# Kernel optimization log

Measured on AMD Instinct MI355X. Metric: run time of the kernel, lower is better.

Reference implementation:

```python
import jax, jax.numpy as jnp
import numpy as np
from jax import lax

B = 4096
SRC = 50   # source_seq_len (encoder runs SRC-1 steps)
TGT = 25   # target_seq_len
R = 1024   # rnn_size
H = 67     # HUMAN_SIZE
I = 82     # input_size = 67 + 15 one-hot actions


def gru_cell(x, h, Wi, Wh, bi, bh):
    # torch.nn.GRUCell semantics; gate order (r, z, n); Wi:[3R,in], Wh:[3R,R]
    gi = x @ Wi.T + bi
    gh = h @ Wh.T + bh
    ir, iz, inn = jnp.split(gi, 3, axis=1)
    hr, hz, hn = jnp.split(gh, 3, axis=1)
    r = jax.nn.sigmoid(ir + hr)
    z = jax.nn.sigmoid(iz + hz)
    n = jnp.tanh(inn + r * hn)
    return (1.0 - z) * n + z * h


def setup_inputs() -> dict:
    key = jax.random.key(0)
    ks = jax.random.split(key, 12)
    s = 0.05
    return {
        "encoder_inputs": jax.random.normal(ks[0], (B, SRC - 1, I), jnp.float32),
        "decoder_inputs": jax.random.normal(ks[1], (B, TGT, I), jnp.float32),
        "Wi1": jax.random.normal(ks[2], (3 * R, I), jnp.float32) * s,
        "Wh1": jax.random.normal(ks[3], (3 * R, R), jnp.float32) * s,
        "bi1": jax.random.normal(ks[4], (3 * R,), jnp.float32) * s,
        "bh1": jax.random.normal(ks[5], (3 * R,), jnp.float32) * s,
        "Wi2": jax.random.normal(ks[6], (3 * R, R), jnp.float32) * s,
        "Wh2": jax.random.normal(ks[7], (3 * R, R), jnp.float32) * s,
        "bi2": jax.random.normal(ks[8], (3 * R,), jnp.float32) * s,
        "bh2": jax.random.normal(ks[9], (3 * R,), jnp.float32) * s,
        "Wfc": jax.random.normal(ks[10], (H, 2 * R), jnp.float32) * s,
        "bfc": jax.random.normal(ks[11], (H,), jnp.float32) * s,
        "use_cuda": 0,
    }


def reference(encoder_inputs, decoder_inputs, Wi1, Wh1, bi1, bh1,
              Wi2, Wh2, bi2, bh2, Wfc, bfc, use_cuda):
    # dropout=0.0 / eval mode -> dropout is identity (faithful to module defaults)
    bsz = encoder_inputs.shape[0]
    enc = jnp.transpose(encoder_inputs, (1, 0, 2))  # [SRC-1, B, I]
    dec = jnp.transpose(decoder_inputs, (1, 0, 2))  # [TGT,   B, I]

    s1 = jnp.zeros((bsz, R), encoder_inputs.dtype)
    s2 = jnp.zeros((bsz, R), encoder_inputs.dtype)

    def enc_step(carry, x):
        s1, s2 = carry
        s1 = gru_cell(x, s1, Wi1, Wh1, bi1, bh1)
        s2 = gru_cell(s1, s2, Wi2, Wh2, bi2, bh2)
        return (s1, s2), None

    (s1, s2), _ = lax.scan(enc_step, (s1, s2), enc)

    # decoder feeds back previous output (loop_function = identity on prev)
    prev0 = dec[0][:, :H]

    def dec_step(carry, dec_t):
        s1, s2, prev = carry
        inp = lax.stop_gradient(jnp.concatenate([prev, dec_t[:, H:]], axis=1))  # .detach()
        s1 = gru_cell(inp, s1, Wi1, Wh1, bi1, bh1)
        s2 = gru_cell(s1, s2, Wi2, Wh2, bi2, bh2)
        state_out = jnp.concatenate([s1, s2], axis=1)          # [B, 2R]
        out = inp[:, :H] + state_out @ Wfc.T + bfc             # residual velocities
        return (s1, s2, out), out

    _, outputs = lax.scan(dec_step, (s1, s2, prev0), dec)      # [TGT, B, H]
    return jnp.transpose(outputs, (1, 0, 2))                   # [B, TGT, H]
```

## Files before the change

### kernel.cpp

```cpp
#include <hip/hip_runtime.h>
#include <hip/hip_bf16.h>
#include <math.h>

#define B_        4096
#define ENC_STEPS 49
#define TGT_      25
#define R_        1024
#define H_        67
#define I_        82
#define IP_       96
#define IP2_      192
#define NG_       3072
#define FCN_      128
#define K2_       2048

typedef unsigned short u16;
typedef __attribute__((ext_vector_type(8))) short bf16x8_t;
typedef __attribute__((ext_vector_type(4))) float f32x4_t;

__device__ __forceinline__ float bf2f(u16 h) {
    union { unsigned int u; float f; } v; v.u = ((unsigned int)h) << 16; return v.f;
}
__device__ __forceinline__ u16 f2bf(float f) {
    union { unsigned int u; float f; } v; v.f = f;
    unsigned int u = v.u;
    u += 0x7fffu + ((u >> 16) & 1u);
    return (u16)(u >> 16);
}
__device__ __forceinline__ float sigmf(float x) { return 1.f / (1.f + __expf(-x)); }
__device__ __forceinline__ float tanhfast(float x) { return 1.f - 2.f / (__expf(2.f * x) + 1.f); }

__device__ __forceinline__ void g2l16(const u16* g, u16* l) {
    __builtin_amdgcn_global_load_lds(
        (const __attribute__((address_space(1))) unsigned int*)(const void*)g,
        (__attribute__((address_space(3))) unsigned int*)(void*)l,
        16, 0, 0);
}

__global__ void cast_bf16_kernel(const float* __restrict__ s, u16* __restrict__ d, int n) {
    int i = blockIdx.x * 256 + threadIdx.x;
    if (i < n) d[i] = f2bf(s[i]);
}
__global__ void pad_wi1_dup_kernel(const float* __restrict__ s, u16* __restrict__ d) {
    int i = blockIdx.x * 256 + threadIdx.x;
    if (i >= NG_ * IP2_) return;
    int r = i / IP2_, c = i % IP2_;
    int cc = (c < IP_) ? c : c - IP_;
    d[i] = (cc < I_) ? f2bf(s[r * I_ + cc]) : (u16)0;
}
__global__ void pad_wfc_kernel(const float* __restrict__ s, u16* __restrict__ d) {
    int i = blockIdx.x * 256 + threadIdx.x;
    if (i >= FCN_ * K2_) return;
    int r = i / K2_, c = i % K2_;
    d[i] = (r < H_) ? f2bf(s[r * K2_ + c]) : (u16)0;
}

__global__ void pad_all_x_kernel(const float* __restrict__ enc, u16* __restrict__ xall) {
    int i = blockIdx.x * 256 + threadIdx.x;
    if (i >= B_ * ENC_STEPS * IP_) return;
    int c = i % IP_;
    int t = (i / IP_) % ENC_STEPS;
    int b = i / (IP_ * ENC_STEPS);
    float v = (c < I_) ? enc[((size_t)b * ENC_STEPS + t) * I_ + c] : 0.f;
    u16 hi = f2bf(v);
    u16 lo = f2bf(v - bf2f(hi));
    size_t base = ((size_t)t * B_ + b) * IP2_;
    xall[base + c]       = hi;
    xall[base + IP_ + c] = lo;
}

__global__ void build_inp_kernel(const float* __restrict__ prev, int pstride,
                                 const float* __restrict__ dec, int t,
                                 u16* __restrict__ xpad) {
    int i = blockIdx.x * 256 + threadIdx.x;
    if (i >= B_ * IP_) return;
    int b = i / IP_, c = i % IP_;
    float v = 0.f;
    if (c < H_)      v = prev[(size_t)b * pstride + c];
    else if (c < I_) v = dec[((size_t)b * TGT_ + t) * I_ + c];
    u16 hi = f2bf(v);
    u16 lo = f2bf(v - bf2f(hi));
    xpad[(size_t)b * IP2_ + c]       = hi;
    xpad[(size_t)b * IP2_ + IP_ + c] = lo;
}

template<int KX>
__global__ __launch_bounds__(256, 2) void gru_step_kernel(
    const u16* __restrict__ Ax, int ldax,
    const u16* __restrict__ Wx,
    const u16* __restrict__ Ah, int ldah,
    const u16* __restrict__ Wh,
    const float* __restrict__ bi, const float* __restrict__ bh,
    float* __restrict__ hf,
    u16* __restrict__ hout)
{
    __shared__ __align__(16) u16 As[128 * 32];
    __shared__ __align__(16) u16 Ws[3 * 64 * 32];

    const int tid  = threadIdx.x;
    const int lane = tid & 63, wave = tid >> 6;
    const int wm = wave >> 1, wn = wave & 1;
    const int mbase = blockIdx.y * 128;
    const int nbase = blockIdx.x * 64;
    const int lr = lane & 15;
    const int sw = (((lane >> 4) ^ (lr & 3)) * 8);

    f32x4_t acc_r[4][2], acc_z[4][2], acc_xn[4][2], acc_hn[4][2];
#pragma unroll
    for (int i = 0; i < 4; i++)
#pragma unroll
        for (int j = 0; j < 2; j++) {
            acc_r[i][j]  = (f32x4_t){0,0,0,0};
            acc_z[i][j]  = (f32x4_t){0,0,0,0};
            acc_xn[i][j] = (f32x4_t){0,0,0,0};
            acc_hn[i][j] = (f32x4_t){0,0,0,0};
        }

    for (int k0 = 0; k0 < KX; k0 += 32) {
        __syncthreads();
#pragma unroll
        for (int p = 0; p < 2; p++) {
            int g = tid + p * 256;
            int row = g >> 2;
            int ch  = (g & 3) ^ (row & 3);
            g2l16(Ax + (size_t)(mbase + row) * ldax + k0 + ch * 8, As + g * 8);
        }
#pragma unroll
        for (int p = 0; p < 3; p++) {
            int q = tid + p * 256;
            int gate = q >> 8, rg = (q >> 2) & 63, cw = (q & 3) ^ (rg & 3);
            g2l16(Wx + ((size_t)gate * R_ + nbase + rg) * KX + k0 + cw * 8, Ws + q * 8);
        }
        __syncthreads();
        bf16x8_t a_f[4], w_r[2], w_z[2], w_n[2];
#pragma unroll
        for (int i = 0; i < 4; i++)
            a_f[i] = *(const bf16x8_t*)(As + (wm * 64 + i * 16 + lr) * 32 + sw);
#pragma unroll
        for (int j = 0; j < 2; j++) {
            int c = wn * 32 + j * 16 + lr;
            w_r[j] = *(const bf16x8_t*)(Ws + c * 32 + sw);
            w_z[j] = *(const bf16x8_t*)(Ws + (64 + c) * 32 + sw);
            w_n[j] = *(const bf16x8_t*)(Ws + (128 + c) * 32 + sw);
        }
#pragma unroll
        for (int i = 0; i < 4; i++)
#pragma unroll
            for (int j = 0; j < 2; j++) {
                acc_r[i][j]  = __builtin_amdgcn_mfma_f32_16x16x32_bf16(a_f[i], w_r[j], acc_r[i][j], 0, 0, 0);
                acc_z[i][j]  = __builtin_amdgcn_mfma_f32_16x16x32_bf16(a_f[i], w_z[j], acc_z[i][j], 0, 0, 0);
                acc_xn[i][j] = __builtin_amdgcn_mfma_f32_16x16x32_bf16(a_f[i], w_n[j], acc_xn[i][j], 0, 0, 0);
            }
    }

    for (int k0 = 0; k0 < R_; k0 += 32) {
        __syncthreads();
#pragma unroll
        for (int p = 0; p < 2; p++) {
            int g = tid + p * 256;
            int row = g >> 2;
            int ch  = (g & 3) ^ (row & 3);
            g2l16(Ah + (size_t)(mbase + row) * ldah + k0 + ch * 8, As + g * 8);
        }
#pragma unroll
        for (int p = 0; p < 3; p++) {
            int q = tid + p * 256;
            int gate = q >> 8, rg = (q >> 2) & 63, cw = (q & 3) ^ (rg & 3);
            g2l16(Wh + ((size_t)gate * R_ + nbase + rg) * R_ + k0 + cw * 8, Ws + q * 8);
        }
        __syncthreads();
        bf16x8_t a_f[4], w_r[2], w_z[2], w_n[2];
#pragma unroll
        for (int i = 0; i < 4; i++)
            a_f[i] = *(const bf16x8_t*)(As + (wm * 64 + i * 16 + lr) * 32 + sw);
#pragma unroll
        for (int j = 0; j < 2; j++) {
            int c = wn * 32 + j * 16 + lr;
            w_r[j] = *(const bf16x8_t*)(Ws + c * 32 + sw);
            w_z[j] = *(const bf16x8_t*)(Ws + (64 + c) * 32 + sw);
            w_n[j] = *(const bf16x8_t*)(Ws + (128 + c) * 32 + sw);
        }
#pragma unroll
        for (int i = 0; i < 4; i++)
#pragma unroll
            for (int j = 0; j < 2; j++) {
                acc_r[i][j]  = __builtin_amdgcn_mfma_f32_16x16x32_bf16(a_f[i], w_r[j], acc_r[i][j], 0, 0, 0);
                acc_z[i][j]  = __builtin_amdgcn_mfma_f32_16x16x32_bf16(a_f[i], w_z[j], acc_z[i][j], 0, 0, 0);
                acc_hn[i][j] = __builtin_amdgcn_mfma_f32_16x16x32_bf16(a_f[i], w_n[j], acc_hn[i][j], 0, 0, 0);
            }
    }

    const int rr2 = (lane >> 4) * 4;
#pragma unroll
    for (int j = 0; j < 2; j++) {
        const int col = nbase + wn * 32 + j * 16 + lr;
        const float b_ir = bi[col],          b_hr = bh[col];
        const float b_iz = bi[R_ + col],     b_hz = bh[R_ + col];
        const float b_in = bi[2 * R_ + col], b_hn = bh[2 * R_ + col];
#pragma unroll
        for (int i = 0; i < 4; i++) {
#pragma unroll
            for (int r = 0; r < 4; r++) {
                const int row = mbase + wm * 64 + i * 16 + rr2 + r;
                const float hold = hf[(size_t)row * R_ + col];
                const float rv = sigmf(acc_r[i][j][r] + b_ir + b_hr);
                const float zv = sigmf(acc_z[i][j][r] + b_iz + b_hz);
                const float nv = tanhfast(acc_xn[i][j][r] + b_in + rv * (acc_hn[i][j][r] + b_hn));
                const float hn = (1.f - zv) * nv + zv * hold;
                hf[(size_t)row * R_ + col] = hn;
                hout[(size_t)row * K2_ + col] = f2bf(hn);
            }
        }
    }
}

__global__ __launch_bounds__(256) void fc_part_kernel(
    const u16* __restrict__ A, const u16* __restrict__ W, float* __restrict__ part) {
    __shared__ __align__(16) u16 As[64 * 32];
    __shared__ __align__(16) u16 Bs[128 * 32];
    const int tid  = threadIdx.x;
    const int lane = tid & 63, wave = tid >> 6;
    const int wm = wave >> 1, wn = wave & 1;
    const int mbase = blockIdx.y * 64;
    const int kbase = blockIdx.x * 512;
    const int lr = lane & 15, lk = (lane >> 4) * 8;

    f32x4_t acc[2][4];
#pragma unroll
    for (int i = 0; i < 2; i++)
#pragma unroll
        for (int j = 0; j < 4; j++) acc[i][j] = (f32x4_t){0, 0, 0, 0};

    for (int k0 = 0; k0 < 512; k0 += 32) {
        __syncthreads();
        {
            int g = tid;
            g2l16(A + (size_t)(mbase + (g >> 2)) * K2_ + kbase + k0 + (g & 3) * 8, As + g * 8);
        }
#pragma unroll
        for (int p = 0; p < 2; p++) {
            int q = tid + p * 256;
            g2l16(W + (size_t)(q >> 2) * K2_ + kbase + k0 + (q & 3) * 8, Bs + q * 8);
        }
        __syncthreads();
        bf16x8_t a_f[2], b_f[4];
#pragma unroll
        for (int i = 0; i < 2; i++)
            a_f[i] = *(const bf16x8_t*)(As + (wm * 32 + i * 16 + lr) * 32 + lk);
#pragma unroll
        for (int j = 0; j < 4; j++)
            b_f[j] = *(const bf16x8_t*)(Bs + (wn * 64 + j * 16 + lr) * 32 + lk);
#pragma unroll
        for (int i = 0; i < 2; i++)
#pragma unroll
            for (int j = 0; j < 4; j++)
                acc[i][j] = __builtin_amdgcn_mfma_f32_16x16x32_bf16(a_f[i], b_f[j], acc[i][j], 0, 0, 0);
    }
    const int rr2 = (lane >> 4) * 4;
#pragma unroll
    for (int i = 0; i < 2; i++)
#pragma unroll
        for (int r = 0; r < 4; r++) {
            int row = mbase + wm * 32 + i * 16 + rr2 + r;
#pragma unroll
            for (int j = 0; j < 4; j++) {
                int col = wn * 64 + j * 16 + lr;
                part[((size_t)blockIdx.x * B_ + row) * FCN_ + col] = acc[i][j][r];
            }
        }
}

__global__ void fc_finish_kernel(const float* __restrict__ part, const float* __restrict__ prev,
                                 int pstride, const float* __restrict__ bfc,
                                 float* __restrict__ out, int t,
                                 const float* __restrict__ dec, u16* __restrict__ xpad,
                                 int write_x) {
    int i = blockIdx.x * 256 + threadIdx.x;
    if (i >= B_ * IP_) return;
    int b = i / IP_, c = i % IP_;
    float v = 0.f;
    if (c < H_) {
        size_t idx = (size_t)b * FCN_ + c;
        const size_t S = (size_t)B_ * FCN_;
        float s = (part[idx] + part[S + idx]) + (part[2 * S + idx] + part[3 * S + idx]);
        v = prev[(size_t)b * pstride + c] + s + bfc[c];
        out[((size_t)b * TGT_ + t) * H_ + c] = v;
    } else if (c < I_ && write_x) {
        v = dec[((size_t)b * TGT_ + (t + 1)) * I_ + c];
    }
    if (write_x) {
        u16 hi = f2bf(v);
        u16 lo = f2bf(v - bf2f(hi));
        xpad[(size_t)b * IP2_ + c]       = hi;
        xpad[(size_t)b * IP2_ + IP_ + c] = lo;
    }
}

extern "C" void kernel_launch(void* const* d_in, const int* in_sizes, int n_in,
                              void* d_out, int out_size, void* d_ws, size_t ws_size,
                              hipStream_t stream) {
    (void)in_sizes; (void)n_in; (void)out_size; (void)ws_size;
    const float* enc = (const float*)d_in[0];
    const float* dec = (const float*)d_in[1];
    const float* Wi1 = (const float*)d_in[2];
    const float* Wh1 = (const float*)d_in[3];
    const float* bi1 = (const float*)d_in[4];
    const float* bh1 = (const float*)d_in[5];
    const float* Wi2 = (const float*)d_in[6];
    const float* Wh2 = (const float*)d_in[7];
    const float* bi2 = (const float*)d_in[8];
    const float* bh2 = (const float*)d_in[9];
    const float* Wfc = (const float*)d_in[10];
    const float* bfc = (const float*)d_in[11];
    float* out = (float*)d_out;

    char* ws = (char*)d_ws;
    size_t off = 0;
    auto alloc = [&](size_t bytes) -> char* {
        char* p = ws + off;
        off += (bytes + 255) & ~(size_t)255;
        return p;
    };
    u16* Wh1b  = (u16*)alloc((size_t)NG_ * R_ * 2);
    u16* Wi2b  = (u16*)alloc((size_t)NG_ * R_ * 2);
    u16* Wh2b  = (u16*)alloc((size_t)NG_ * R_ * 2);
    u16* Wi1pb = (u16*)alloc((size_t)NG_ * IP2_ * 2);
    u16* Wfcb  = (u16*)alloc((size_t)FCN_ * K2_ * 2);
    u16* sbuf0 = (u16*)alloc((size_t)B_ * K2_ * 2);
    float* s1f = (float*)alloc((size_t)B_ * R_ * 4);
    float* s2f = (float*)alloc((size_t)B_ * R_ * 4);
    u16* sbuf1 = (u16*)alloc((size_t)B_ * K2_ * 2);
    u16* xall  = (u16*)alloc((size_t)ENC_STEPS * B_ * IP2_ * 2);
    u16* xpad2 = (u16*)alloc((size_t)B_ * IP2_ * 2);
    float* cfcp = (float*)alloc((size_t)4 * B_ * FCN_ * 4);
    u16* sbuf[2] = { sbuf0, sbuf1 };

    hipMemsetAsync(sbuf0, 0,
                   (size_t)B_ * K2_ * 2 + 2 * (size_t)B_ * R_ * 4, stream);

    cast_bf16_kernel<<<(NG_ * R_ + 255) / 256, 256, 0, stream>>>(Wh1, Wh1b, NG_ * R_);
    cast_bf16_kernel<<<(NG_ * R_ + 255) / 256, 256, 0, stream>>>(Wi2, Wi2b, NG_ * R_);
    cast_bf16_kernel<<<(NG_ * R_ + 255) / 256, 256, 0, stream>>>(Wh2, Wh2b, NG_ * R_);
    pad_wi1_dup_kernel<<<(NG_ * IP2_ + 255) / 256, 256, 0, stream>>>(Wi1, Wi1pb);
    pad_wfc_kernel<<<(FCN_ * K2_ + 255) / 256, 256, 0, stream>>>(Wfc, Wfcb);
    pad_all_x_kernel<<<(B_ * ENC_STEPS * IP_ + 255) / 256, 256, 0, stream>>>(enc, xall);

    dim3 gru_grid(R_ / 64, B_ / 128, 1);
    dim3 fc_grid(4, B_ / 64, 1);
    const int binp_blocks = (B_ * IP_ + 255) / 256;
    const int fcf_blocks  = (B_ * IP_ + 255) / 256;

    int phase = 0;

    for (int t = 0; t < ENC_STEPS; t++) {
        u16* cur = sbuf[phase];
        u16* nxt = sbuf[phase ^ 1];
        gru_step_kernel<IP2_><<<gru_grid, 256, 0, stream>>>(
            xall + (size_t)t * B_ * IP2_, IP2_, Wi1pb,
            cur, K2_, Wh1b, bi1, bh1, s1f, nxt);
        gru_step_kernel<R_><<<gru_grid, 256, 0, stream>>>(
            nxt, K2_, Wi2b,
            cur + R_, K2_, Wh2b, bi2, bh2, s2f, nxt + R_);
        phase ^= 1;
    }

    build_inp_kernel<<<binp_blocks, 256, 0, stream>>>(dec, TGT_ * I_, dec, 0, xpad2);
    for (int t = 0; t < TGT_; t++) {
        const float* prev;
        int pstride;
        if (t == 0) { prev = dec;                 pstride = TGT_ * I_; }
        else        { prev = out + (t - 1) * H_;  pstride = TGT_ * H_; }
        u16* cur = sbuf[phase];
        u16* nxt = sbuf[phase ^ 1];
        gru_step_kernel<IP2_><<<gru_grid, 256, 0, stream>>>(
            xpad2, IP2_, Wi1pb,
            cur, K2_, Wh1b, bi1, bh1, s1f, nxt);
        gru_step_kernel<R_><<<gru_grid, 256, 0, stream>>>(
            nxt, K2_, Wi2b,
            cur + R_, K2_, Wh2b, bi2, bh2, s2f, nxt + R_);
        fc_part_kernel<<<fc_grid, 256, 0, stream>>>(nxt, Wfcb, cfcp);
        fc_finish_kernel<<<fcf_blocks, 256, 0, stream>>>(
            cfcp, prev, pstride, bfc, out, t, dec, xpad2, (t < TGT_ - 1) ? 1 : 0);
        phase ^= 1;
    }
}
```

Measured before the change: 8.599 ms.

## Triple-buffer GRU step K-loop with async prefetch and adjust LDS swizzle

Merges the input and hidden K-loops of the GRU step kernel into one loop that triple-buffers the A and W tiles in LDS. It prefetches two stages ahead, using vmcnt waits and one barrier per stage in place of two syncthreads per iteration. It also raises wave priority around the MFMA block, and switches the LDS XOR swizzle to use row>>1 in both the GRU and FC kernels to reduce bank conflicts. LDS use triples, to about 48KB per block, which may limit the two-blocks-per-CU occupancy target.

```diff
diff --git a/kernel.cpp b/kernel.cpp
--- a/kernel.cpp
+++ b/kernel.cpp
@@ -94,8 +94,8 @@
     float* __restrict__ hf,
     u16* __restrict__ hout)
 {
-    __shared__ __align__(16) u16 As[128 * 32];
-    __shared__ __align__(16) u16 Ws[3 * 64 * 32];
+    __shared__ __align__(16) u16 As[3][128 * 32];
+    __shared__ __align__(16) u16 Ws[3][3 * 64 * 32];
 
     const int tid  = threadIdx.x;
     const int lane = tid & 63, wave = tid >> 6;
@@ -103,7 +103,10 @@
     const int mbase = blockIdx.y * 128;
     const int nbase = blockIdx.x * 64;
     const int lr = lane & 15;
-    const int sw = (((lane >> 4) ^ (lr & 3)) * 8);
+    const int sw = (((lane >> 4) ^ ((lr >> 1) & 3)) * 8);
+
+    constexpr int NX = KX / 32;
+    constexpr int NT = NX + R_ / 32;
 
     f32x4_t acc_r[4][2], acc_z[4][2], acc_xn[4][2], acc_hn[4][2];
 #pragma unroll
@@ -116,78 +119,80 @@
             acc_hn[i][j] = (f32x4_t){0,0,0,0};
         }
 
-    for (int k0 = 0; k0 < KX; k0 += 32) {
-        __syncthreads();
+    auto stage = [&](int s, int b) {
+        const u16* A; int lda; const u16* W; int ldw; int k0;
+        if (s < NX) { A = Ax; lda = ldax; W = Wx; ldw = KX; k0 = s * 32; }
+        else        { A = Ah; lda = ldah; W = Wh; ldw = R_;  k0 = (s - NX) * 32; }
 #pragma unroll
         for (int p = 0; p < 2; p++) {
             int g = tid + p * 256;
             int row = g >> 2;
-            int ch  = (g & 3) ^ (row & 3);
-            g2l16(Ax + (size_t)(mbase + row) * ldax + k0 + ch * 8, As + g * 8);
+            int ch  = (g & 3) ^ ((row >> 1) & 3);
+            g2l16(A + (size_t)(mbase + row) * lda + k0 + ch * 8, As[b] + g * 8);
         }
 #pragma unroll
         for (int p = 0; p < 3; p++) {
             int q = tid + p * 256;
-            int gate = q >> 8, rg = (q >> 2) & 63, cw = (q & 3) ^ (rg & 3);
-            g2l16(Wx + ((size_t)gate * R_ + nbase + rg) * KX + k0 + cw * 8, Ws + q * 8);
-        }
-        __syncthreads();
+            int row = q >> 2;
+            int gate = q >> 8, rg = (q >> 2) & 63;
+            int cw = (q & 3) ^ ((row >> 1) & 3);
+            g2l16(W + ((size_t)gate * R_ + nbase + rg) * ldw + k0 + cw * 8, Ws[b] + q * 8);
+        }
+    };
+
+    auto compute = [&](int s, int b) {
         bf16x8_t a_f[4], w_r[2], w_z[2], w_n[2];
 #pragma unroll
         for (int i = 0; i < 4; i++)
-            a_f[i] = *(const bf16x8_t*)(As + (wm * 64 + i * 16 + lr) * 32 + sw);
+            a_f[i] = *(const bf16x8_t*)(As[b] + (wm * 64 + i * 16 + lr) * 32 + sw);
 #pragma unroll
         for (int j = 0; j < 2; j++) {
             int c = wn * 32 + j * 16 + lr;
-            w_r[j] = *(const bf16x8_t*)(Ws + c * 32 + sw);
-            w_z[j] = *(const bf16x8_t*)(Ws + (64 + c) * 32 + sw);
-            w_n[j] = *(const bf16x8_t*)(Ws + (128 + c) * 32 + sw);
-        }
+            w_r[j] = *(const bf16x8_t*)(Ws[b] + c * 32 + sw);
+            w_z[j] = *(const bf16x8_t*)(Ws[b] + (64 + c) * 32 + sw);
+            w_n[j] = *(const bf16x8_t*)(Ws[b] + (128 + c) * 32 + sw);
+        }
+        __builtin_amdgcn_s_setprio(1);
 #pragma unroll
         for (int i = 0; i < 4; i++)
 #pragma unroll
             for (int j = 0; j < 2; j++) {
-                acc_r[i][j]  = __builtin_amdgcn_mfma_f32_16x16x32_bf16(a_f[i], w_r[j], acc_r[i][j], 0, 0, 0);
-                acc_z[i][j]  = __builtin_amdgcn_mfma_f32_16x16x32_bf16(a_f[i], w_z[j], acc_z[i][j], 0, 0, 0);
-                acc_xn[i][j] = __builtin_amdgcn_mfma_f32_16x16x32_bf16(a_f[i], w_n[j], acc_xn[i][j], 0, 0, 0);
+                acc_r[i][j] = __builtin_amdgcn_mfma_f32_16x16x32_bf16(a_f[i], w_r[j], acc_r[i][j], 0, 0, 0);
+                acc_z[i][j] = __builtin_amdgcn_mfma_f32_16x16x32_bf16(a_f[i], w_z[j], acc_z[i][j], 0, 0, 0);
             }
-    }
-
-    for (int k0 = 0; k0 < R_; k0 += 32) {
-        __syncthreads();
-#pragma unroll
-        for (int p = 0; p < 2; p++) {
-            int g = tid + p * 256;
-            int row = g >> 2;
-            int ch  = (g & 3) ^ (row & 3);
-            g2l16(Ah + (size_t)(mbase + row) * ldah + k0 + ch * 8, As + g * 8);
-        }
-#pragma unroll
-        for (int p = 0; p < 3; p++) {
-            int q = tid + p * 256;
-            int gate = q >> 8, rg = (q >> 2) & 63, cw = (q & 3) ^ (rg & 3);
-            g2l16(Wh + ((size_t)gate * R_ + nbase + rg) * R_ + k0 + cw * 8, Ws + q * 8);
-        }
-        __syncthreads();
-        bf16x8_t a_f[4], w_r[2], w_z[2], w_n[2];
-#pragma unroll
-        for (int i = 0; i < 4; i++)
-            a_f[i] = *(const bf16x8_t*)(As + (wm * 64 + i * 16 + lr) * 32 + sw);
-#pragma unroll
-        for (int j = 0; j < 2; j++) {
-            int c = wn * 32 + j * 16 + lr;
-            w_r[j] = *(const bf16x8_t*)(Ws + c * 32 + sw);
-            w_z[j] = *(const bf16x8_t*)(Ws + (64 + c) * 32 + sw);
-            w_n[j] = *(const bf16x8_t*)(Ws + (128 + c) * 32 + sw);
-        }
-#pragma unroll
-        for (int i = 0; i < 4; i++)
-#pragma unroll
-            for (int j = 0; j < 2; j++) {
-                acc_r[i][j]  = __builtin_amdgcn_mfma_f32_16x16x32_bf16(a_f[i], w_r[j], acc_r[i][j], 0, 0, 0);
-                acc_z[i][j]  = __builtin_amdgcn_mfma_f32_16x16x32_bf16(a_f[i], w_z[j], acc_z[i][j], 0, 0, 0);
-                acc_hn[i][j] = __builtin_amdgcn_mfma_f32_16x16x32_bf16(a_f[i], w_n[j], acc_hn[i][j], 0, 0, 0);
-            }
+        if (s < NX) {
+#pragma unroll
+            for (int i = 0; i < 4; i++)
+#pragma unroll
+                for (int j = 0; j < 2; j++)
+                    acc_xn[i][j] = __builtin_amdgcn_mfma_f32_16x16x32_bf16(a_f[i], w_n[j], acc_xn[i][j], 0, 0, 0);
+        } else {
+#pragma unroll
+            for (int i = 0; i < 4; i++)
+#pragma unroll
+                for (int j = 0; j < 2; j++)
+                    acc_hn[i][j] = __builtin_amdgcn_mfma_f32_16x16x32_bf16(a_f[i], w_n[j], acc_hn[i][j], 0, 0, 0);
+        }
+        __builtin_amdgcn_s_setprio(0);
+    };
+
+    stage(0, 0);
+    stage(1, 1);
+    int b = 0;
+    for (int s = 0; s < NT; ++s) {
+        if (s + 2 < NT) {
+            asm volatile("s_waitcnt vmcnt(5)" ::: "memory");
+            __builtin_amdgcn_s_barrier();
+            __builtin_amdgcn_sched_barrier(0);
+            int b2 = b + 2; if (b2 >= 3) b2 -= 3;
+            stage(s + 2, b2);
+        } else {
+            asm volatile("s_waitcnt vmcnt(0)" ::: "memory");
+            __builtin_amdgcn_s_barrier();
+            __builtin_amdgcn_sched_barrier(0);
+        }
+        compute(s, b);
+        if (++b == 3) b = 0;
     }
 
     const int rr2 = (lane >> 4) * 4;
@@ -223,7 +228,8 @@
     const int wm = wave >> 1, wn = wave & 1;
     const int mbase = blockIdx.y * 64;
     const int kbase = blockIdx.x * 512;
-    const int lr = lane & 15, lk = (lane >> 4) * 8;
+    const int lr = lane & 15;
+    const int sw = (((lane >> 4) ^ ((lr >> 1) & 3)) * 8);
 
     f32x4_t acc[2][4];
 #pragma unroll
@@ -235,21 +241,25 @@
         __syncthreads();
         {
             int g = tid;
-            g2l16(A + (size_t)(mbase + (g >> 2)) * K2_ + kbase + k0 + (g & 3) * 8, As + g * 8);
+            int row = g >> 2;
+            int ch  = (g & 3) ^ ((row >> 1) & 3);
+            g2l16(A + (size_t)(mbase + row) * K2_ + kbase + k0 + ch * 8, As + g * 8);
         }
 #pragma unroll
         for (int p = 0; p < 2; p++) {
             int q = tid + p * 256;
-            g2l16(W + (size_t)(q >> 2) * K2_ + kbase + k0 + (q & 3) * 8, Bs + q * 8);
+            int row = q >> 2;
+            int cw  = (q & 3) ^ ((row >> 1) & 3);
+            g2l16(W + (size_t)row * K2_ + kbase + k0 + cw * 8, Bs + q * 8);
         }
         __syncthreads();
         bf16x8_t a_f[2], b_f[4];
 #pragma unroll
         for (int i = 0; i < 2; i++)
-            a_f[i] = *(const bf16x8_t*)(As + (wm * 32 + i * 16 + lr) * 32 + lk);
+            a_f[i] = *(const bf16x8_t*)(As + (wm * 32 + i * 16 + lr) * 32 + sw);
 #pragma unroll
         for (int j = 0; j < 4; j++)
-            b_f[j] = *(const bf16x8_t*)(Bs + (wn * 64 + j * 16 + lr) * 32 + lk);
+            b_f[j] = *(const bf16x8_t*)(Bs + (wn * 64 + j * 16 + lr) * 32 + sw);
 #pragma unroll
         for (int i = 0; i < 2; i++)
 #pragma unroll
```

Result: slower. 8.817 ms (+2.5%).

## Replace LDS-staged GEMM tiles with direct global-to-register double-buffered loads

Applied to the files above, without the earlier changes.

The GRU step and FC partial kernels no longer stage A and W tiles through shared memory with global_load_lds and two barriers per k-step. Each wave now loads its MFMA fragments straight from global memory into registers, with two register buffers so the next k-slice loads while the current one feeds the MFMAs. The GRU kernel also raises wave priority around the MFMA blocks. This removes the barriers and LDS traffic, but tiles shared between waves are no longer reused through LDS, so global and L2 traffic rises and register pressure grows under launch_bounds(256,2).

```diff
diff --git a/kernel.cpp b/kernel.cpp
--- a/kernel.cpp
+++ b/kernel.cpp
@@ -30,13 +30,6 @@
 __device__ __forceinline__ float sigmf(float x) { return 1.f / (1.f + __expf(-x)); }
 __device__ __forceinline__ float tanhfast(float x) { return 1.f - 2.f / (__expf(2.f * x) + 1.f); }
 
-__device__ __forceinline__ void g2l16(const u16* g, u16* l) {
-    __builtin_amdgcn_global_load_lds(
-        (const __attribute__((address_space(1))) unsigned int*)(const void*)g,
-        (__attribute__((address_space(3))) unsigned int*)(void*)l,
-        16, 0, 0);
-}
-
 __global__ void cast_bf16_kernel(const float* __restrict__ s, u16* __restrict__ d, int n) {
     int i = blockIdx.x * 256 + threadIdx.x;
     if (i < n) d[i] = f2bf(s[i]);
@@ -94,16 +87,15 @@
     float* __restrict__ hf,
     u16* __restrict__ hout)
 {
-    __shared__ __align__(16) u16 As[128 * 32];
-    __shared__ __align__(16) u16 Ws[3 * 64 * 32];
-
     const int tid  = threadIdx.x;
     const int lane = tid & 63, wave = tid >> 6;
     const int wm = wave >> 1, wn = wave & 1;
     const int mbase = blockIdx.y * 128;
     const int nbase = blockIdx.x * 64;
-    const int lr = lane & 15;
-    const int sw = (((lane >> 4) ^ (lr & 3)) * 8);
+    const int lr = lane & 15, lk = (lane >> 4) * 8;
+
+    constexpr int NX = KX / 32;
+    constexpr int NH = R_ / 32;
 
     f32x4_t acc_r[4][2], acc_z[4][2], acc_xn[4][2], acc_hn[4][2];
 #pragma unroll
@@ -116,79 +108,69 @@
             acc_hn[i][j] = (f32x4_t){0,0,0,0};
         }
 
-    for (int k0 = 0; k0 < KX; k0 += 32) {
-        __syncthreads();
-#pragma unroll
-        for (int p = 0; p < 2; p++) {
-            int g = tid + p * 256;
-            int row = g >> 2;
-            int ch  = (g & 3) ^ (row & 3);
-            g2l16(Ax + (size_t)(mbase + row) * ldax + k0 + ch * 8, As + g * 8);
+    auto run_pass = [&](const u16* A, int lda, const u16* W, int ldw, int nsteps,
+                        f32x4_t (&accn)[4][2]) {
+        const u16* ap[4];
+        const u16* wp[6];
+#pragma unroll
+        for (int i = 0; i < 4; i++)
+            ap[i] = A + (size_t)(mbase + wm * 64 + i * 16 + lr) * lda + lk;
+#pragma unroll
+        for (int g = 0; g < 3; g++)
+#pragma unroll
+            for (int j = 0; j < 2; j++)
+                wp[g * 2 + j] = W + ((size_t)g * R_ + nbase + wn * 32 + j * 16 + lr) * ldw + lk;
+
+        bf16x8_t a0[4], w0[6], a1[4], w1[6];
+        auto ld0 = [&](int k0) {
+#pragma unroll
+            for (int i = 0; i < 4; i++) a0[i] = *(const bf16x8_t*)(ap[i] + k0);
+#pragma unroll
+            for (int i = 0; i < 6; i++) w0[i] = *(const bf16x8_t*)(wp[i] + k0);
+        };
+        auto ld1 = [&](int k0) {
+#pragma unroll
+            for (int i = 0; i < 4; i++) a1[i] = *(const bf16x8_t*)(ap[i] + k0);
+#pragma unroll
+            for (int i = 0; i < 6; i++) w1[i] = *(const bf16x8_t*)(wp[i] + k0);
+        };
+        auto fm0 = [&]() {
+            __builtin_amdgcn_s_setprio(1);
+#pragma unroll
+            for (int i = 0; i < 4; i++)
+#pragma unroll
+                for (int j = 0; j < 2; j++) {
+                    acc_r[i][j] = __builtin_amdgcn_mfma_f32_16x16x32_bf16(a0[i], w0[j],     acc_r[i][j], 0, 0, 0);
+                    acc_z[i][j] = __builtin_amdgcn_mfma_f32_16x16x32_bf16(a0[i], w0[2 + j], acc_z[i][j], 0, 0, 0);
+                    accn[i][j]  = __builtin_amdgcn_mfma_f32_16x16x32_bf16(a0[i], w0[4 + j], accn[i][j], 0, 0, 0);
+                }
+            __builtin_amdgcn_s_setprio(0);
+        };
+        auto fm1 = [&]() {
+            __builtin_amdgcn_s_setprio(1);
+#pragma unroll
+            for (int i = 0; i < 4; i++)
+#pragma unroll
+                for (int j = 0; j < 2; j++) {
+                    acc_r[i][j] = __builtin_amdgcn_mfma_f32_16x16x32_bf16(a1[i], w1[j],     acc_r[i][j], 0, 0, 0);
+                    acc_z[i][j] = __builtin_amdgcn_mfma_f32_16x16x32_bf16(a1[i], w1[2 + j], acc_z[i][j], 0, 0, 0);
+                    accn[i][j]  = __builtin_amdgcn_mfma_f32_16x16x32_bf16(a1[i], w1[4 + j], accn[i][j], 0, 0, 0);
+                }
+            __builtin_amdgcn_s_setprio(0);
+        };
+
+        ld0(0);
+#pragma unroll 1
+        for (int s = 0; s < nsteps; s += 2) {
+            if (s + 1 < nsteps) ld1((s + 1) * 32);
+            fm0();
+            if (s + 2 < nsteps) ld0((s + 2) * 32);
+            if (s + 1 < nsteps) fm1();
         }
-#pragma unroll
-        for (int p = 0; p < 3; p++) {
-            int q = tid + p * 256;
-            int gate = q >> 8, rg = (q >> 2) & 63, cw = (q & 3) ^ (rg & 3);
-            g2l16(Wx + ((size_t)gate * R_ + nbase + rg) * KX + k0 + cw * 8, Ws + q * 8);
-        }
-        __syncthreads();
-        bf16x8_t a_f[4], w_r[2], w_z[2], w_n[2];
-#pragma unroll
-        for (int i = 0; i < 4; i++)
-            a_f[i] = *(const bf16x8_t*)(As + (wm * 64 + i * 16 + lr) * 32 + sw);
-#pragma unroll
-        for (int j = 0; j < 2; j++) {
-            int c = wn * 32 + j * 16 + lr;
-            w_r[j] = *(const bf16x8_t*)(Ws + c * 32 + sw);
-            w_z[j] = *(const bf16x8_t*)(Ws + (64 + c) * 32 + sw);
-            w_n[j] = *(const bf16x8_t*)(Ws + (128 + c) * 32 + sw);
-        }
-#pragma unroll
-        for (int i = 0; i < 4; i++)
-#pragma unroll
-            for (int j = 0; j < 2; j++) {
-                acc_r[i][j]  = __builtin_amdgcn_mfma_f32_16x16x32_bf16(a_f[i], w_r[j], acc_r[i][j], 0, 0, 0);
-                acc_z[i][j]  = __builtin_amdgcn_mfma_f32_16x16x32_bf16(a_f[i], w_z[j], acc_z[i][j], 0, 0, 0);
-                acc_xn[i][j] = __builtin_amdgcn_mfma_f32_16x16x32_bf16(a_f[i], w_n[j], acc_xn[i][j], 0, 0, 0);
-            }
-    }
-
-    for (int k0 = 0; k0 < R_; k0 += 32) {
-        __syncthreads();
-#pragma unroll
-        for (int p = 0; p < 2; p++) {
-            int g = tid + p * 256;
-            int row = g >> 2;
-            int ch  = (g & 3) ^ (row & 3);
-            g2l16(Ah + (size_t)(mbase + row) * ldah + k0 + ch * 8, As + g * 8);
-        }
-#pragma unroll
-        for (int p = 0; p < 3; p++) {
-            int q = tid + p * 256;
-            int gate = q >> 8, rg = (q >> 2) & 63, cw = (q & 3) ^ (rg & 3);
-            g2l16(Wh + ((size_t)gate * R_ + nbase + rg) * R_ + k0 + cw * 8, Ws + q * 8);
-        }
-        __syncthreads();
-        bf16x8_t a_f[4], w_r[2], w_z[2], w_n[2];
-#pragma unroll
-        for (int i = 0; i < 4; i++)
-            a_f[i] = *(const bf16x8_t*)(As + (wm * 64 + i * 16 + lr) * 32 + sw);
-#pragma unroll
-        for (int j = 0; j < 2; j++) {
-            int c = wn * 32 + j * 16 + lr;
-            w_r[j] = *(const bf16x8_t*)(Ws + c * 32 + sw);
-            w_z[j] = *(const bf16x8_t*)(Ws + (64 + c) * 32 + sw);
-            w_n[j] = *(const bf16x8_t*)(Ws + (128 + c) * 32 + sw);
-        }
-#pragma unroll
-        for (int i = 0; i < 4; i++)
-#pragma unroll
-            for (int j = 0; j < 2; j++) {
-                acc_r[i][j]  = __builtin_amdgcn_mfma_f32_16x16x32_bf16(a_f[i], w_r[j], acc_r[i][j], 0, 0, 0);
-                acc_z[i][j]  = __builtin_amdgcn_mfma_f32_16x16x32_bf16(a_f[i], w_z[j], acc_z[i][j], 0, 0, 0);
-                acc_hn[i][j] = __builtin_amdgcn_mfma_f32_16x16x32_bf16(a_f[i], w_n[j], acc_hn[i][j], 0, 0, 0);
-            }
-    }
+    };
+
+    run_pass(Ax, ldax, Wx, KX, NX, acc_xn);
+    run_pass(Ah, ldah, Wh, R_, NH, acc_hn);
 
     const int rr2 = (lane >> 4) * 4;
 #pragma unroll
@@ -216,8 +198,6 @@
 
 __global__ __launch_bounds__(256) void fc_part_kernel(
     const u16* __restrict__ A, const u16* __restrict__ W, float* __restrict__ part) {
-    __shared__ __align__(16) u16 As[64 * 32];
-    __shared__ __align__(16) u16 Bs[128 * 32];
     const int tid  = threadIdx.x;
     const int lane = tid & 63, wave = tid >> 6;
     const int wm = wave >> 1, wn = wave & 1;
@@ -231,31 +211,52 @@
 #pragma unroll
         for (int j = 0; j < 4; j++) acc[i][j] = (f32x4_t){0, 0, 0, 0};
 
-    for (int k0 = 0; k0 < 512; k0 += 32) {
-        __syncthreads();
-        {
-            int g = tid;
-            g2l16(A + (size_t)(mbase + (g >> 2)) * K2_ + kbase + k0 + (g & 3) * 8, As + g * 8);
-        }
-#pragma unroll
-        for (int p = 0; p < 2; p++) {
-            int q = tid + p * 256;
-            g2l16(W + (size_t)(q >> 2) * K2_ + kbase + k0 + (q & 3) * 8, Bs + q * 8);
-        }
-        __syncthreads();
-        bf16x8_t a_f[2], b_f[4];
+    const u16* ap[2];
+    const u16* bp[4];
+#pragma unroll
+    for (int i = 0; i < 2; i++)
+        ap[i] = A + (size_t)(mbase + wm * 32 + i * 16 + lr) * K2_ + kbase + lk;
+#pragma unroll
+    for (int j = 0; j < 4; j++)
+        bp[j] = W + (size_t)(wn * 64 + j * 16 + lr) * K2_ + kbase + lk;
+
+    bf16x8_t a0[2], b0[4], a1[2], b1[4];
+    auto ld0 = [&](int k0) {
+#pragma unroll
+        for (int i = 0; i < 2; i++) a0[i] = *(const bf16x8_t*)(ap[i] + k0);
+#pragma unroll
+        for (int j = 0; j < 4; j++) b0[j] = *(const bf16x8_t*)(bp[j] + k0);
+    };
+    auto ld1 = [&](int k0) {
+#pragma unroll
+        for (int i = 0; i < 2; i++) a1[i] = *(const bf16x8_t*)(ap[i] + k0);
+#pragma unroll
+        for (int j = 0; j < 4; j++) b1[j] = *(const bf16x8_t*)(bp[j] + k0);
+    };
+    auto fm0 = [&]() {
 #pragma unroll
         for (int i = 0; i < 2; i++)
-            a_f[i] = *(const bf16x8_t*)(As + (wm * 32 + i * 16 + lr) * 32 + lk);
-#pragma unroll
-        for (int j = 0; j < 4; j++)
-            b_f[j] = *(const bf16x8_t*)(Bs + (wn * 64 + j * 16 + lr) * 32 + lk);
+#pragma unroll
+            for (int j = 0; j < 4; j++)
+                acc[i][j] = __builtin_amdgcn_mfma_f32_16x16x32_bf16(a0[i], b0[j], acc[i][j], 0, 0, 0);
+    };
+    auto fm1 = [&]() {
 #pragma unroll
         for (int i = 0; i < 2; i++)
 #pragma unroll
             for (int j = 0; j < 4; j++)
-                acc[i][j] = __builtin_amdgcn_mfma_f32_16x16x32_bf16(a_f[i], b_f[j], acc[i][j], 0, 0, 0);
-    }
+                acc[i][j] = __builtin_amdgcn_mfma_f32_16x16x32_bf16(a1[i], b1[j], acc[i][j], 0, 0, 0);
+    };
+
+    ld0(0);
+#pragma unroll 1
+    for (int s = 0; s < 16; s += 2) {
+        if (s + 1 < 16) ld1((s + 1) * 32);
+        fm0();
+        if (s + 2 < 16) ld0((s + 2) * 32);
+        if (s + 1 < 16) fm1();
+    }
+
     const int rr2 = (lane >> 4) * 4;
 #pragma unroll
     for (int i = 0; i < 2; i++)
```

New measurement: 18.44 ms. 114% more time.
